# Kernel optimization log

Measured on AMD Instinct MI355X. Metric: run time of the kernel, lower is better.

Reference implementation:

```python
import jax, jax.numpy as jnp
import numpy as np

HEAD_COUNT = 16
HEAD_DIM = 128  # embed_count // head_count = 2048 // 16


def setup_inputs() -> dict:
    key = jax.random.key(0)
    k0, k1, k2, k3, k4 = jax.random.split(key, 5)
    B, C, S = 4, 2048, 1024
    keys = jax.random.normal(k0, (B, C, 1, S), dtype=jnp.float32)
    values = jax.random.normal(k1, (B, C, 1, S), dtype=jnp.float32)
    queries = jax.random.normal(k2, (B, C, 1, S), dtype=jnp.float32)
    attention_mask = jax.random.randint(k3, (B, S), 0, 2).astype(bool)
    # guarantee at least one valid key per batch row so softmax is finite
    attention_mask = attention_mask.at[:, 0].set(True)
    w_out = jax.random.normal(k4, (C, C), dtype=jnp.float32) * 0.02
    return {"keys": keys, "values": values, "queries": queries,
            "attention_mask": attention_mask, "w_out": w_out}


def reference(keys, values, queries, attention_mask, w_out):
    B, C, _, S = keys.shape
    h, d = HEAD_COUNT, HEAD_DIM
    # keys: [B,C,1,S] -> transpose(1,3) -> [B,S,1,C] -> [B,S,h,d]
    k = jnp.transpose(keys[:, :, 0, :], (0, 2, 1)).reshape(B, S, h, d)      # bkhd
    # values/queries: [B,C,1,S] -> [B,h,d,S] -> transpose(1,2) -> [B,d,h,S]
    v = jnp.transpose(values[:, :, 0, :].reshape(B, h, d, S), (0, 2, 1, 3))  # bdhk
    q = jnp.transpose(queries[:, :, 0, :].reshape(B, h, d, S), (0, 2, 1, 3)) # bdhq
    # additive mask bias: 0 where attended, -inf where masked; broadcast over h,q
    bias = jnp.where(attention_mask, 0.0, -jnp.inf).astype(keys.dtype)       # [B,K]
    scale = 1.0 / np.sqrt(d).astype(np.float32)
    w = jnp.einsum('bdhq,bkhd->bkhq', q * scale, k)                          # [B,K,h,Q]
    w = w + bias[:, :, None, None]
    w = jax.nn.softmax(w, axis=1)  # softmax over keys (dim 1)
    hid = jnp.einsum('bkhq,bdhk->bdhq', w, v)                                # [B,d,h,Q]
    hid = jnp.transpose(hid, (0, 2, 1, 3)).reshape(B, C, S)                  # [B,C,Q]
    out = jnp.einsum('oc,bcq->boq', w_out, hid)                              # 1x1 conv out_proj
    return out.reshape(B, C, 1, S)
```

## Files before the change

### kernel.cpp

```cpp
#include <hip/hip_runtime.h>

#define Bq 4
#define Cc 2048
#define Ss 1024
#define Hh 16
#define Dd 128

#define QSCALE 0.127517429f

typedef __bf16 bf16x8 __attribute__((ext_vector_type(8)));
typedef float  f32x4  __attribute__((ext_vector_type(4)));

__device__ __forceinline__ ushort f2bf(float f) {
    uint u = __float_as_uint(f);
    u += 0x7FFFu + ((u >> 16) & 1u);
    return (ushort)(u >> 16);
}
__device__ __forceinline__ uint pack2bf(float a, float b) {
    return (uint)f2bf(a) | ((uint)f2bf(b) << 16);
}
__device__ __forceinline__ void gld16(const void* g, void* l) {
    __builtin_amdgcn_global_load_lds(
        (const __attribute__((address_space(1))) unsigned int*)g,
        (__attribute__((address_space(3))) unsigned int*)l, 16, 0, 0);
}

__global__ __launch_bounds__(256) void mask_bias_k(const unsigned* __restrict__ mask,
                                                   float* __restrict__ bias) {
    __shared__ int f01, ff;
    const int t = threadIdx.x;
    if (t == 0) { f01 = 0; ff = 0; }
    __syncthreads();
    int a = 0, b = 0;
    for (int i = t; i < 1024; i += 256) {
        unsigned v = mask[i];
        if (v != 0u && v != 1u) a = 1;
        if (v != 0u && v != 0x3F800000u) b = 1;
    }
    if (a) atomicOr(&f01, 1);
    if (b) atomicOr(&ff, 1);
    __syncthreads();
    const int mode = f01 ? (ff ? 1 : 2) : 0;
    const int* mi = (const int*)mask;
    const unsigned char* mb = (const unsigned char*)mask;
    const float* mf = (const float*)mask;
    for (int i = t; i < Bq * Ss; i += 256) {
        bool on;
        if (mode == 0)      on = (mi[i] != 0);
        else if (mode == 1) on = (mb[i] != 0);
        else                on = (mf[i] != 0.0f);
        bias[i] = on ? 0.0f : -1e30f;
    }
}

__global__ __launch_bounds__(256) void wcvt_swz(const float* __restrict__ w,
                                                ushort* __restrict__ wb) {
    const size_t e = ((size_t)blockIdx.x * 256 + threadIdx.x) * 8;
    const int row = (int)(e >> 11), col = (int)(e & 2047);
    const int colS = (col & ~63) | ((col & 63) ^ ((row & 7) << 3));
    float4 v0 = *(const float4*)&w[e];
    float4 v1 = *(const float4*)&w[e + 4];
    uint4 o;
    o.x = pack2bf(v0.x, v0.y); o.y = pack2bf(v0.z, v0.w);
    o.z = pack2bf(v1.x, v1.y); o.w = pack2bf(v1.z, v1.w);
    *(uint4*)&wb[(size_t)row * 2048 + colS] = o;
}

__global__ __launch_bounds__(256) void vcvt_perm(const float* __restrict__ v,
                                                 ushort* __restrict__ vb) {
    const int tid = blockIdx.x * 256 + threadIdx.x;
    const int row = tid >> 7;
    const int cp = tid & 127;
    const int blk = (cp >> 3) * 64;
    const int j0 = cp & 7;
    const int b5 = j0 >> 2, h = j0 & 3;
    const float* src = v + (size_t)row * 1024 + blk + 32 * b5 + 4 * h;
    float4 A = *(const float4*)src;
    float4 B = *(const float4*)(src + 16);
    uint4 o;
    o.x = pack2bf(A.x, A.y); o.y = pack2bf(A.z, A.w);
    o.z = pack2bf(B.x, B.y); o.w = pack2bf(B.z, B.w);
    *(uint4*)&vb[(size_t)row * 1024 + blk + ((j0 * 8) ^ ((row & 7) << 3))] = o;
}

__global__ __launch_bounds__(256) void qk_prep(const float* __restrict__ queries,
                                               const float* __restrict__ keys,
                                               ushort* __restrict__ Qt,
                                               ushort* __restrict__ Kt) {
    __shared__ float T[128][65];
    const int t = threadIdx.x;
    const int s0 = blockIdx.x * 64;
    const int bh = blockIdx.y;
    const int isK = blockIdx.z;
    const float* src = (isK ? keys : queries) + (size_t)bh * 128 * 1024;
    const float sc = isK ? 1.0f : QSCALE;

#pragma unroll
    for (int p = 0; p < 8; ++p) {
        const int d = p * 16 + (t >> 4);
        float4 v = *(const float4*)&src[(size_t)d * 1024 + s0 + (t & 15) * 4];
        T[d][(t & 15) * 4 + 0] = v.x * sc;
        T[d][(t & 15) * 4 + 1] = v.y * sc;
        T[d][(t & 15) * 4 + 2] = v.z * sc;
        T[d][(t & 15) * 4 + 3] = v.w * sc;
    }
    __syncthreads();

    ushort* outp = isK ? Kt : Qt;
#pragma unroll
    for (int p = 0; p < 4; ++p) {
        const int k = p * 16 + (t >> 4);
        const int x = t & 15;
        uint4 o;
        o.x = pack2bf(T[x * 8 + 0][k], T[x * 8 + 1][k]);
        o.y = pack2bf(T[x * 8 + 2][k], T[x * 8 + 3][k]);
        o.z = pack2bf(T[x * 8 + 4][k], T[x * 8 + 5][k]);
        o.w = pack2bf(T[x * 8 + 6][k], T[x * 8 + 7][k]);
        const size_t rowbyte = ((size_t)bh * 1024 + s0 + k) * 256;
        const int boff = isK ? ((x * 16) ^ ((k & 7) << 4)) : (x * 16);
        *(uint4*)((char*)outp + rowbyte + boff) = o;
    }
}

__global__ __launch_bounds__(512, 2) void attn5(const ushort* __restrict__ Qt,
                                                const ushort* __restrict__ Kt,
                                                const ushort* __restrict__ Vbf,
                                                const float* __restrict__ bias,
                                                ushort* __restrict__ hidT) {
    __shared__ __align__(16) char SMEM[102400];
    float* biasS = (float*)(SMEM + 98304);

    const int t = threadIdx.x, l = t & 63, w = t >> 6;
    const int kk = l & 15, g = l >> 4;

    const int bid = blockIdx.x;
    const int vid = (bid & 7) * 32 + (bid >> 3);
    const int bh = vid >> 2, qt = vid & 3;
    const int b = bh >> 4;
    const int q0 = qt * 256;
    const size_t bhbase = (size_t)bh * 1024;

    for (int i = t; i < Ss; i += 512) biasS[i] = bias[b * Ss + i];

    bf16x8 qf[2][4];
#pragma unroll
    for (int qs = 0; qs < 2; ++qs) {
        const ushort* qrow = Qt + (bhbase + q0 + w * 32 + qs * 16 + kk) * 128;
#pragma unroll
        for (int dc = 0; dc < 4; ++dc)
            qf[qs][dc] = *(const bf16x8*)(qrow + dc * 32 + g * 8);
    }

    float lrun[2] = {0.0f, 0.0f};
    f32x4 hacc[2][8];
#pragma unroll
    for (int qs = 0; qs < 2; ++qs)
#pragma unroll
        for (int i = 0; i < 8; ++i) hacc[qs][i] = (f32x4){0.f, 0.f, 0.f, 0.f};

#define ATTN_STAGE(bufi, cki)                                                   \
    {                                                                           \
        const int k0n = (cki) * 64;                                             \
        ushort* Kd = (ushort*)SMEM + (bufi) * 8192;                             \
        ushort* Vd = (ushort*)(SMEM + 49152) + (bufi) * 8192;                   \
        _Pragma("unroll")                                                       \
        for (int ii = 0; ii < 4; ++ii) {                                        \
            const int inst = ii * 8 + w;                                        \
            if (inst < 16) {                                                    \
                gld16(Kt + (bhbase + k0n + inst * 4 + (l >> 4)) * 128 +         \
                          (l & 15) * 8,                                         \
                      Kd + inst * 512);                                         \
            } else {                                                            \
                const int i2 = inst - 16;                                       \
                gld16(Vbf + ((size_t)bh * 128 + i2 * 8 + (l >> 3)) * 1024 +     \
                          k0n + (l & 7) * 8,                                    \
                      Vd + i2 * 512);                                           \
            }                                                                   \
        }                                                                       \
    }

#define ATTN_COMPUTE(bi, ck)                                                     \
    {                                                                            \
        const int k0 = (ck) * 64;                                                \
        const ushort* KTb = (const ushort*)SMEM + (bi) * 8192;                   \
        const ushort* Vsb = (const ushort*)(SMEM + 49152) + (bi) * 8192;         \
        f32x4 sc[2][4];                                                          \
        __builtin_amdgcn_s_setprio(1);                                           \
        _Pragma("unroll")                                                        \
        for (int ns = 0; ns < 4; ++ns) {                                         \
            bf16x8 kf[4];                                                        \
            const ushort* kr = KTb + (ns * 16 + kk) * 128;                       \
            _Pragma("unroll")                                                    \
            for (int dc = 0; dc < 4; ++dc)                                       \
                kf[dc] = *(const bf16x8*)(kr +                                   \
                             ((dc * 32 + g * 8) ^ ((kk & 7) << 3)));             \
            _Pragma("unroll")                                                    \
            for (int qs = 0; qs < 2; ++qs) {                                     \
                f32x4 a = (f32x4){0.f, 0.f, 0.f, 0.f};                           \
                _Pragma("unroll")                                                \
                for (int dc = 0; dc < 4; ++dc)                                   \
                    a = __builtin_amdgcn_mfma_f32_16x16x32_bf16(                 \
                        kf[dc], qf[qs][dc], a, 0, 0, 0);                         \
                sc[qs][ns] = a;                                                  \
            }                                                                    \
        }                                                                        \
        __builtin_amdgcn_s_setprio(0);                                           \
        float4 bk4[4];                                                           \
        _Pragma("unroll")                                                        \
        for (int ns = 0; ns < 4; ++ns)                                           \
            bk4[ns] = *(const float4*)&biasS[k0 + ns * 16 + g * 4];              \
        bf16x8 pb[2][2];                                                         \
        _Pragma("unroll")                                                        \
        for (int qs = 0; qs < 2; ++qs) {                                         \
            float pv[4][4];                                                      \
            float s = 0.0f;                                                      \
            _Pragma("unroll")                                                    \
            for (int ns = 0; ns < 4; ++ns) {                                     \
                const float* bb2 = (const float*)&bk4[ns];                       \
                _Pragma("unroll")                                                \
                for (int r = 0; r < 4; ++r) {                                    \
                    float p = exp2f(sc[qs][ns][r] + bb2[r]);                     \
                    pv[ns][r] = p;                                               \
                    s += p;                                                      \
                }                                                                \
            }                                                                    \
            lrun[qs] += s;                                                       \
            _Pragma("unroll")                                                    \
            for (int kh = 0; kh < 2; ++kh) {                                     \
                bf16x8 vpk;                                                      \
                _Pragma("unroll")                                                \
                for (int j = 0; j < 8; ++j)                                      \
                    vpk[j] = (__bf16)pv[2 * kh + (j >> 2)][j & 3];               \
                pb[qs][kh] = vpk;                                                \
            }                                                                    \
        }                                                                        \
        __builtin_amdgcn_s_setprio(1);                                           \
        _Pragma("unroll")                                                        \
        for (int kh = 0; kh < 2; ++kh) {                                         \
            _Pragma("unroll")                                                    \
            for (int ds = 0; ds < 8; ++ds) {                                     \
                bf16x8 vf = *(const bf16x8*)(Vsb + (ds * 16 + kk) * 64 +         \
                                 ((kh * 32 + g * 8) ^ ((kk & 7) << 3)));         \
                hacc[0][ds] = __builtin_amdgcn_mfma_f32_16x16x32_bf16(           \
                    vf, pb[0][kh], hacc[0][ds], 0, 0, 0);                        \
                hacc[1][ds] = __builtin_amdgcn_mfma_f32_16x16x32_bf16(           \
                    vf, pb[1][kh], hacc[1][ds], 0, 0, 0);                        \
            }                                                                    \
        }                                                                        \
        __builtin_amdgcn_s_setprio(0);                                           \
    }

    ATTN_STAGE(0, 0);
    ATTN_STAGE(1, 1);
    asm volatile("s_waitcnt vmcnt(4)" ::: "memory");
    __builtin_amdgcn_s_barrier();

    int cb = 0, sb = 2;
    for (int ck = 0; ck < 14; ++ck) {
        ATTN_STAGE(sb, ck + 2);
        ATTN_COMPUTE(cb, ck);
        asm volatile("s_waitcnt vmcnt(4)" ::: "memory");
        __builtin_amdgcn_s_barrier();
        cb = (cb == 2) ? 0 : cb + 1;
        sb = (sb == 2) ? 0 : sb + 1;
    }
    ATTN_COMPUTE(cb, 14);
    asm volatile("s_waitcnt vmcnt(0)" ::: "memory");
    __builtin_amdgcn_s_barrier();
    cb = (cb == 2) ? 0 : cb + 1;
    ATTN_COMPUTE(cb, 15);
#undef ATTN_STAGE
#undef ATTN_COMPUTE

    float linv[2];
#pragma unroll
    for (int qs = 0; qs < 2; ++qs) {
        float s = lrun[qs];
        s += __shfl_xor(s, 16);
        s += __shfl_xor(s, 32);
        linv[qs] = 1.0f / s;
    }

    __syncthreads();
    {
        ushort* hs = (ushort*)SMEM;
#pragma unroll
        for (int qs = 0; qs < 2; ++qs) {
            const int row = w * 32 + qs * 16 + kk;
#pragma unroll
            for (int ds = 0; ds < 8; ++ds) {
                uint2 pk;
                pk.x = pack2bf(hacc[qs][ds][0] * linv[qs], hacc[qs][ds][1] * linv[qs]);
                pk.y = pack2bf(hacc[qs][ds][2] * linv[qs], hacc[qs][ds][3] * linv[qs]);
                const int off = row * 256 + ((ds * 32 + g * 8) ^ ((row & 7) << 4));
                *(uint2*)((char*)hs + off) = pk;
            }
        }
    }
    __syncthreads();

    const int hh = bh & 15;
    const char* hsb = (const char*)SMEM;
#pragma unroll
    for (int it = 0; it < 8; ++it) {
        const int idx = it * 512 + t;
        const int q = idx >> 4, x = idx & 15;
        uint4 vv = *(const uint4*)(hsb + q * 256 + x * 16);
        *(uint4*)((char*)hidT + ((size_t)(b * Ss + q0 + q)) * 4096 + hh * 256 + x * 16) = vv;
    }
}

__global__ __launch_bounds__(512, 2) void proj3(const ushort* __restrict__ Wbf,
                                                const ushort* __restrict__ hidT,
                                                float* __restrict__ out) {
    __shared__ __align__(16) char SMEM[147456];
    const int t = threadIdx.x, l = t & 63, w = t >> 6;
    const int kk = l & 15, g = l >> 4;
    const int wr = w >> 1, wc = w & 1;

    const int bid = blockIdx.x;
    const int vid = (bid & 7) * 32 + (bid >> 3);
    const int o0 = (vid >> 5) * 256;
    const int n0 = (vid & 31) * 128;

    f32x4 acc[4][4];
#pragma unroll
    for (int i = 0; i < 4; ++i)
#pragma unroll
        for (int j = 0; j < 4; ++j) acc[i][j] = (f32x4){0.f, 0.f, 0.f, 0.f};

#define PROJ_STAGE(bufi, ks)                                                       \
    {                                                                              \
        ushort* Wd = (ushort*)SMEM + (bufi) * 16384;                               \
        ushort* Hd = (ushort*)(SMEM + 98304) + (bufi) * 8192;                      \
        _Pragma("unroll")                                                          \
        for (int ii = 0; ii < 6; ++ii) {                                           \
            const int inst = ii * 8 + w;                                           \
            if (inst < 32) {                                                       \
                gld16(Wbf + ((size_t)(o0 + inst * 8 + (l >> 3)) * 2048) +          \
                          (ks) * 64 + (l & 7) * 8,                                 \
                      Wd + inst * 512);                                            \
            } else {                                                               \
                const int j = inst - 32;                                           \
                gld16(hidT + ((size_t)(n0 + j * 8 + (l >> 3)) * 2048) +            \
                          (ks) * 64 + (l & 7) * 8,                                 \
                      Hd + j * 512);                                               \
            }                                                                      \
        }                                                                          \
    }

#define PROJ_COMPUTE(bi)                                                           \
    {                                                                              \
        const ushort* Wb2 = (const ushort*)SMEM + (bi) * 16384;                    \
        const ushort* Hb2 = (const ushort*)(SMEM + 98304) + (bi) * 8192;           \
        _Pragma("unroll")                                                          \
        for (int dc = 0; dc < 2; ++dc) {                                           \
            bf16x8 af[4], bf[4];                                                   \
            _Pragma("unroll")                                                      \
            for (int ms = 0; ms < 4; ++ms) {                                       \
                const int row = wr * 64 + ms * 16 + kk;                            \
                af[ms] = *(const bf16x8*)&Wb2[row * 64 +                           \
                             ((dc * 32 + g * 8) ^ ((kk & 7) << 3))];               \
            }                                                                      \
            _Pragma("unroll")                                                      \
            for (int ns = 0; ns < 4; ++ns) {                                       \
                const int row = wc * 64 + ns * 16 + kk;                            \
                bf[ns] = *(const bf16x8*)&Hb2[row * 64 +                           \
                             ((dc * 32 + g * 8) ^ ((kk & 7) << 3))];               \
            }                                                                      \
            __builtin_amdgcn_s_setprio(1);                                         \
            _Pragma("unroll")                                                      \
            for (int ms = 0; ms < 4; ++ms)                                         \
                _Pragma("unroll")                                                  \
                for (int ns = 0; ns < 4; ++ns)                                     \
                    acc[ms][ns] = __builtin_amdgcn_mfma_f32_16x16x32_bf16(         \
                        af[ms], bf[ns], acc[ms][ns], 0, 0, 0);                     \
            __builtin_amdgcn_s_setprio(0);                                         \
        }                                                                          \
    }

    PROJ_STAGE(0, 0);
    PROJ_STAGE(1, 1);
    asm volatile("s_waitcnt vmcnt(6)" ::: "memory");
    __builtin_amdgcn_s_barrier();

    int cb = 0, sbuf = 2;
    for (int ks = 0; ks < 30; ++ks) {
        PROJ_STAGE(sbuf, ks + 2);
        PROJ_COMPUTE(cb);
        asm volatile("s_waitcnt vmcnt(6)" ::: "memory");
        __builtin_amdgcn_s_barrier();
        cb = (cb == 2) ? 0 : cb + 1;
        sbuf = (sbuf == 2) ? 0 : sbuf + 1;
    }
    PROJ_COMPUTE(cb);
    asm volatile("s_waitcnt vmcnt(0)" ::: "memory");
    __builtin_amdgcn_s_barrier();
    cb = (cb == 2) ? 0 : cb + 1;
    PROJ_COMPUTE(cb);
#undef PROJ_STAGE
#undef PROJ_COMPUTE

#pragma unroll
    for (int ms = 0; ms < 4; ++ms)
#pragma unroll
        for (int ns = 0; ns < 4; ++ns) {
            const int o = o0 + wr * 64 + ms * 16 + g * 4;
            const int n = n0 + wc * 64 + ns * 16 + kk;
            const int bb = n >> 10, qq = n & 1023;
            float* op = out + ((size_t)(bb * Cc + o)) * Ss + qq;
#pragma unroll
            for (int r = 0; r < 4; ++r) op[(size_t)r * Ss] = acc[ms][ns][r];
        }
}

extern "C" void kernel_launch(void* const* d_in, const int* in_sizes, int n_in,
                              void* d_out, int out_size, void* d_ws, size_t ws_size,
                              hipStream_t stream) {
    const float*    keys    = (const float*)d_in[0];
    const float*    values  = (const float*)d_in[1];
    const float*    queries = (const float*)d_in[2];
    const unsigned* mask    = (const unsigned*)d_in[3];
    const float*    w_out   = (const float*)d_in[4];
    float* out = (float*)d_out;

    char* ws = (char*)d_ws;
    float*  bias = (float*)ws;
    ushort* Wbf  = (ushort*)(ws + 16384);
    ushort* Qt   = (ushort*)(ws + 16384 + (8u << 20));
    ushort* Kt   = (ushort*)(ws + 16384 + (24u << 20));
    ushort* Vbf  = (ushort*)(ws + 16384 + (40u << 20));
    ushort* hidT = (ushort*)(ws + 16384 + (56u << 20));

    hipLaunchKernelGGL(mask_bias_k, dim3(1), dim3(256), 0, stream, mask, bias);
    hipLaunchKernelGGL(wcvt_swz, dim3(2048), dim3(256), 0, stream, w_out, Wbf);
    hipLaunchKernelGGL(vcvt_perm, dim3(4096), dim3(256), 0, stream, values, Vbf);
    hipLaunchKernelGGL(qk_prep, dim3(16, 64, 2), dim3(256), 0, stream,
                       queries, keys, Qt, Kt);
    hipLaunchKernelGGL(attn5, dim3(256), dim3(512), 0, stream,
                       Qt, Kt, Vbf, bias, hidT);
    hipLaunchKernelGGL(proj3, dim3(256), dim3(512), 0, stream,
                       Wbf, hidT, out);
}
```

Before: 125.7 us.

## Fold mask bias into MFMA accumulator init and restructure projection GEMM pipeline

In the attention kernel, the mask bias now seeds each QK MFMA accumulator, so the separate bias loads and per-element adds before exp2 go away. The projection kernel changes its block tile from 256x128 to 128x256 with a 2x4 wave grid. Its K-loop is split into four sub-steps, one per N sub-tile, each interleaving a slice of the global-to-LDS staging with the MFMAs for that sub-tile. The intent is finer overlap of loads and compute, at the cost of many more barriers per iteration.

```diff
diff --git a/kernel.cpp b/kernel.cpp
--- a/kernel.cpp
+++ b/kernel.cpp
@@ -122,7 +122,7 @@
     }
 }
 
-__global__ __launch_bounds__(512, 2) void attn5(const ushort* __restrict__ Qt,
+__global__ __launch_bounds__(512, 2) void attn6(const ushort* __restrict__ Qt,
                                                 const ushort* __restrict__ Kt,
                                                 const ushort* __restrict__ Vbf,
                                                 const float* __restrict__ bias,
@@ -188,6 +188,7 @@
         __builtin_amdgcn_s_setprio(1);                                           \
         _Pragma("unroll")                                                        \
         for (int ns = 0; ns < 4; ++ns) {                                         \
+            const f32x4 ci = *(const f32x4*)&biasS[k0 + ns * 16 + g * 4];        \
             bf16x8 kf[4];                                                        \
             const ushort* kr = KTb + (ns * 16 + kk) * 128;                       \
             _Pragma("unroll")                                                    \
@@ -196,7 +197,7 @@
                              ((dc * 32 + g * 8) ^ ((kk & 7) << 3)));             \
             _Pragma("unroll")                                                    \
             for (int qs = 0; qs < 2; ++qs) {                                     \
-                f32x4 a = (f32x4){0.f, 0.f, 0.f, 0.f};                           \
+                f32x4 a = ci;                                                    \
                 _Pragma("unroll")                                                \
                 for (int dc = 0; dc < 4; ++dc)                                   \
                     a = __builtin_amdgcn_mfma_f32_16x16x32_bf16(                 \
@@ -205,10 +206,6 @@
             }                                                                    \
         }                                                                        \
         __builtin_amdgcn_s_setprio(0);                                           \
-        float4 bk4[4];                                                           \
-        _Pragma("unroll")                                                        \
-        for (int ns = 0; ns < 4; ++ns)                                           \
-            bk4[ns] = *(const float4*)&biasS[k0 + ns * 16 + g * 4];              \
         bf16x8 pb[2][2];                                                         \
         _Pragma("unroll")                                                        \
         for (int qs = 0; qs < 2; ++qs) {                                         \
@@ -216,10 +213,9 @@
             float s = 0.0f;                                                      \
             _Pragma("unroll")                                                    \
             for (int ns = 0; ns < 4; ++ns) {                                     \
-                const float* bb2 = (const float*)&bk4[ns];                       \
                 _Pragma("unroll")                                                \
                 for (int r = 0; r < 4; ++r) {                                    \
-                    float p = exp2f(sc[qs][ns][r] + bb2[r]);                     \
+                    float p = exp2f(sc[qs][ns][r]);                              \
                     pv[ns][r] = p;                                               \
                     s += p;                                                      \
                 }                                                                \
@@ -310,18 +306,18 @@
     }
 }
 
-__global__ __launch_bounds__(512, 2) void proj3(const ushort* __restrict__ Wbf,
+__global__ __launch_bounds__(512, 2) void proj4(const ushort* __restrict__ Wbf,
                                                 const ushort* __restrict__ hidT,
                                                 float* __restrict__ out) {
     __shared__ __align__(16) char SMEM[147456];
     const int t = threadIdx.x, l = t & 63, w = t >> 6;
     const int kk = l & 15, g = l >> 4;
-    const int wr = w >> 1, wc = w & 1;
+    const int wr = w >> 2, wc = w & 3;
 
     const int bid = blockIdx.x;
     const int vid = (bid & 7) * 32 + (bid >> 3);
-    const int o0 = (vid >> 5) * 256;
-    const int n0 = (vid & 31) * 128;
+    const int o0 = (vid & 15) * 128;
+    const int n0 = (vid >> 4) * 256;
 
     f32x4 acc[4][4];
 #pragma unroll
@@ -329,77 +325,99 @@
 #pragma unroll
         for (int j = 0; j < 4; ++j) acc[i][j] = (f32x4){0.f, 0.f, 0.f, 0.f};
 
-#define PROJ_STAGE(bufi, ks)                                                       \
-    {                                                                              \
-        ushort* Wd = (ushort*)SMEM + (bufi) * 16384;                               \
-        ushort* Hd = (ushort*)(SMEM + 98304) + (bufi) * 8192;                      \
-        _Pragma("unroll")                                                          \
-        for (int ii = 0; ii < 6; ++ii) {                                           \
-            const int inst = ii * 8 + w;                                           \
-            if (inst < 32) {                                                       \
-                gld16(Wbf + ((size_t)(o0 + inst * 8 + (l >> 3)) * 2048) +          \
-                          (ks) * 64 + (l & 7) * 8,                                 \
-                      Wd + inst * 512);                                            \
-            } else {                                                               \
-                const int j = inst - 32;                                           \
-                gld16(hidT + ((size_t)(n0 + j * 8 + (l >> 3)) * 2048) +            \
-                          (ks) * 64 + (l & 7) * 8,                                 \
-                      Hd + j * 512);                                               \
-            }                                                                      \
-        }                                                                          \
-    }
-
-#define PROJ_COMPUTE(bi)                                                           \
-    {                                                                              \
-        const ushort* Wb2 = (const ushort*)SMEM + (bi) * 16384;                    \
-        const ushort* Hb2 = (const ushort*)(SMEM + 98304) + (bi) * 8192;           \
-        _Pragma("unroll")                                                          \
-        for (int dc = 0; dc < 2; ++dc) {                                           \
-            bf16x8 af[4], bf[4];                                                   \
-            _Pragma("unroll")                                                      \
-            for (int ms = 0; ms < 4; ++ms) {                                       \
-                const int row = wr * 64 + ms * 16 + kk;                            \
-                af[ms] = *(const bf16x8*)&Wb2[row * 64 +                           \
-                             ((dc * 32 + g * 8) ^ ((kk & 7) << 3))];               \
-            }                                                                      \
-            _Pragma("unroll")                                                      \
-            for (int ns = 0; ns < 4; ++ns) {                                       \
-                const int row = wc * 64 + ns * 16 + kk;                            \
-                bf[ns] = *(const bf16x8*)&Hb2[row * 64 +                           \
-                             ((dc * 32 + g * 8) ^ ((kk & 7) << 3))];               \
-            }                                                                      \
-            __builtin_amdgcn_s_setprio(1);                                         \
-            _Pragma("unroll")                                                      \
-            for (int ms = 0; ms < 4; ++ms)                                         \
-                _Pragma("unroll")                                                  \
-                for (int ns = 0; ns < 4; ++ns)                                     \
-                    acc[ms][ns] = __builtin_amdgcn_mfma_f32_16x16x32_bf16(         \
-                        af[ms], bf[ns], acc[ms][ns], 0, 0, 0);                     \
-            __builtin_amdgcn_s_setprio(0);                                         \
-        }                                                                          \
-    }
-
-    PROJ_STAGE(0, 0);
-    PROJ_STAGE(1, 1);
+    const int swz = ((kk & 7) << 3);
+
+#define P4_STAGE_A(st, ks)                                                      \
+    {                                                                           \
+        ushort* Ad = (ushort*)SMEM + (st) * 8192;                               \
+        _Pragma("unroll")                                                       \
+        for (int ii = 0; ii < 2; ++ii) {                                        \
+            const int i = ii * 8 + w;                                           \
+            gld16(Wbf + (size_t)(o0 + i * 8 + (l >> 3)) * 2048 + (ks) * 64 +    \
+                      (l & 7) * 8,                                              \
+                  Ad + i * 512);                                                \
+        }                                                                       \
+    }
+#define P4_STAGE_B(st, ks, jj0)                                                 \
+    {                                                                           \
+        ushort* Bd = (ushort*)(SMEM + 49152) + (st) * 16384;                    \
+        _Pragma("unroll")                                                       \
+        for (int jj = (jj0); jj < (jj0) + 2; ++jj) {                            \
+            const int j = jj * 8 + w;                                           \
+            gld16(hidT + (size_t)(n0 + j * 8 + (l >> 3)) * 2048 + (ks) * 64 +   \
+                      (l & 7) * 8,                                              \
+                  Bd + j * 512);                                                \
+        }                                                                       \
+    }
+#define P4_MFMA(nsv)                                                            \
+    __builtin_amdgcn_s_setprio(1);                                              \
+    _Pragma("unroll")                                                           \
+    for (int dc = 0; dc < 2; ++dc)                                              \
+        _Pragma("unroll")                                                       \
+        for (int ms = 0; ms < 4; ++ms)                                          \
+            acc[ms][nsv] = __builtin_amdgcn_mfma_f32_16x16x32_bf16(             \
+                af[dc][ms], bfr[dc], acc[ms][nsv], 0, 0, 0);                    \
+    __builtin_amdgcn_s_setprio(0);
+#define P4_BF(nsv)                                                              \
+    _Pragma("unroll")                                                           \
+    for (int dc = 0; dc < 2; ++dc)                                              \
+        bfr[dc] = *(const bf16x8*)&Bb[(wc * 64 + (nsv) * 16 + kk) * 64 +        \
+                                      ((dc * 32 + g * 8) ^ swz)];
+#define P4_BAR()  __builtin_amdgcn_s_barrier()
+#define P4_LGKM() asm volatile("s_waitcnt lgkmcnt(0)" ::: "memory")
+
+    P4_STAGE_A(0, 0); P4_STAGE_B(0, 0, 0); P4_STAGE_B(0, 0, 2);
+    P4_STAGE_A(1, 1); P4_STAGE_B(1, 1, 0); P4_STAGE_B(1, 1, 2);
     asm volatile("s_waitcnt vmcnt(6)" ::: "memory");
-    __builtin_amdgcn_s_barrier();
-
-    int cb = 0, sbuf = 2;
-    for (int ks = 0; ks < 30; ++ks) {
-        PROJ_STAGE(sbuf, ks + 2);
-        PROJ_COMPUTE(cb);
-        asm volatile("s_waitcnt vmcnt(6)" ::: "memory");
-        __builtin_amdgcn_s_barrier();
-        cb = (cb == 2) ? 0 : cb + 1;
-        sbuf = (sbuf == 2) ? 0 : sbuf + 1;
-    }
-    PROJ_COMPUTE(cb);
-    asm volatile("s_waitcnt vmcnt(0)" ::: "memory");
-    __builtin_amdgcn_s_barrier();
-    cb = (cb == 2) ? 0 : cb + 1;
-    PROJ_COMPUTE(cb);
-#undef PROJ_STAGE
-#undef PROJ_COMPUTE
+    P4_BAR();
+
+    int ct = 0, st = 2;
+    for (int tt = 0; tt < 32; ++tt) {
+        const ushort* Ab = (const ushort*)SMEM + ct * 8192;
+        const ushort* Bb = (const ushort*)(SMEM + 49152) + ct * 16384;
+        const int ksS = tt + 2;
+        bf16x8 af[2][4], bfr[2];
+
+#pragma unroll
+        for (int dc = 0; dc < 2; ++dc)
+#pragma unroll
+            for (int ms = 0; ms < 4; ++ms)
+                af[dc][ms] = *(const bf16x8*)&Ab[(wr * 64 + ms * 16 + kk) * 64 +
+                                                 ((dc * 32 + g * 8) ^ swz)];
+        P4_BF(0);
+        if (tt < 30) P4_STAGE_A(st, ksS);
+        P4_BAR(); P4_LGKM();
+        P4_MFMA(0);
+        P4_BAR();
+
+        P4_BF(1);
+        if (tt < 30) P4_STAGE_B(st, ksS, 0);
+        P4_BAR(); P4_LGKM();
+        P4_MFMA(1);
+        P4_BAR();
+
+        P4_BF(2);
+        if (tt < 30) P4_STAGE_B(st, ksS, 2);
+        P4_BAR(); P4_LGKM();
+        P4_MFMA(2);
+        P4_BAR();
+
+        P4_BF(3);
+        if (tt < 30)       { asm volatile("s_waitcnt vmcnt(6)" ::: "memory"); }
+        else if (tt == 30) { asm volatile("s_waitcnt vmcnt(0)" ::: "memory"); }
+        P4_BAR(); P4_LGKM();
+        P4_MFMA(3);
+        P4_BAR();
+
+        ct = (ct == 2) ? 0 : ct + 1;
+        st = (st == 2) ? 0 : st + 1;
+    }
+#undef P4_STAGE_A
+#undef P4_STAGE_B
+#undef P4_MFMA
+#undef P4_BF
+#undef P4_BAR
+#undef P4_LGKM
 
 #pragma unroll
     for (int ms = 0; ms < 4; ++ms)
@@ -437,8 +455,8 @@
     hipLaunchKernelGGL(vcvt_perm, dim3(4096), dim3(256), 0, stream, values, Vbf);
     hipLaunchKernelGGL(qk_prep, dim3(16, 64, 2), dim3(256), 0, stream,
                        queries, keys, Qt, Kt);
-    hipLaunchKernelGGL(attn5, dim3(256), dim3(512), 0, stream,
+    hipLaunchKernelGGL(attn6, dim3(256), dim3(512), 0, stream,
                        Qt, Kt, Vbf, bias, hidT);
-    hipLaunchKernelGGL(proj3, dim3(256), dim3(512), 0, stream,
+    hipLaunchKernelGGL(proj4, dim3(256), dim3(512), 0, stream,
                        Wbf, hidT, out);
 }
```

Result: no change. 128.1 us (+1.9%).
